# Performance work log

Measured on AMD Instinct MI355X. Metric: run time of the kernel, lower is better.

## Reference

```python
import jax, jax.numpy as jnp
import numpy as np

DIM = 1024
N_HEAD = 16
SEQ = 2048
GATE_IN = 12
ROPE_BASE = 10000.0
ATTN_SCALE = 0.1
EPS = 1e-6


def setup_inputs() -> dict:
    key = jax.random.key(0)
    ks = jax.random.split(key, 8)
    std = 0.5 * DIM ** -0.5
    bound = (3.0 ** 0.5) * std
    x = jax.random.normal(ks[0], (1, SEQ, DIM), dtype=jnp.float32)
    v1 = jax.random.normal(ks[1], (1, SEQ, DIM), dtype=jnp.float32)
    Wq = jax.random.uniform(ks[2], (DIM, DIM), jnp.float32, -bound, bound)
    Wk = jax.random.uniform(ks[3], (DIM, DIM), jnp.float32, -bound, bound)
    Wv = jax.random.uniform(ks[4], (DIM, DIM), jnp.float32, -bound, bound)
    # original zero-inits c_proj/attn_gate; use small random so output is non-trivial
    Wproj = jax.random.normal(ks[5], (DIM, DIM), dtype=jnp.float32) * 0.02
    Wgate = jax.random.normal(ks[6], (N_HEAD, GATE_IN), dtype=jnp.float32) * 0.02
    lamb = jnp.float32(0.5)
    return {"x": x, "v1": v1, "Wq": Wq, "Wk": Wk, "Wv": Wv,
            "Wproj": Wproj, "lamb": lamb, "Wgate": Wgate}


def _rms_norm(t):
    return t * jax.lax.rsqrt(jnp.mean(jnp.square(t), axis=-1, keepdims=True) + EPS)


def _rotary(t):
    # t: [B, T, H, hd]; rotates halves per the module's sign convention
    B, T, H, hd = t.shape
    d = hd // 2
    inv_freq = 1.0 / (ROPE_BASE ** (jnp.arange(0, hd, 2, dtype=jnp.float32) / hd))  # [d]
    freqs = jnp.arange(T, dtype=jnp.float32)[:, None] * inv_freq[None, :]  # [T, d]
    cos = jnp.cos(freqs)[None, :, None, :]
    sin = jnp.sin(freqs)[None, :, None, :]
    x1, x2 = t[..., :d], t[..., d:]
    y1 = x1 * cos + x2 * sin
    y2 = -x1 * sin + x2 * cos
    return jnp.concatenate([y1, y2], axis=-1)


def reference(x, v1, Wq, Wk, Wv, Wproj, lamb, Wgate):
    B, T, dim = x.shape
    H = Wgate.shape[0]
    hd = dim // H

    q = (x @ Wq.T).reshape(B, T, H, hd)
    k = (x @ Wk.T).reshape(B, T, H, hd)
    v = (x @ Wv.T).reshape(B, T, H, hd)

    # lambda-blended value mixing with residual value stream v1
    v = (1.0 - lamb) * v + lamb * v1.reshape(B, T, H, hd)

    q, k = _rms_norm(q), _rms_norm(k)
    q, k = _rotary(q), _rotary(k)

    # causal attention with fixed scale 0.1 (flex_attention block-sparse causal)
    scores = jnp.einsum("bthd,bshd->bhts", q, k) * ATTN_SCALE  # [B,H,T,T]
    causal = jnp.tril(jnp.ones((T, T), dtype=bool))
    scores = jnp.where(causal[None, None], scores, jnp.float32(-1e30))
    probs = jax.nn.softmax(scores, axis=-1)
    y = jnp.einsum("bhts,bshd->bthd", probs, v)  # [B,T,H,hd]

    # sigmoid gate from the first 12 channels of x, per head
    gate = jax.nn.sigmoid(x[..., :Wgate.shape[1]] @ Wgate.T)[..., None]  # [B,T,H,1]
    y = (y * gate).reshape(B, T, dim)
    y = y @ Wproj.T
    return y, v1
```

## Files before the change

kernel.cpp:

```cpp
#include <hip/hip_runtime.h>
#include <hip/hip_bf16.h>

#define T_SEQ 2048
#define NH 16
#define HD 64
#define SCALE_LOG2E 0.14426950408889634f

typedef __attribute__((ext_vector_type(8))) short bf16x8;
typedef __attribute__((ext_vector_type(4))) short bf16x4;
typedef __attribute__((ext_vector_type(4))) float f32x4;

__device__ __forceinline__ short f2bs(float f) {
  union { float f; unsigned u; } v; v.f = f;
  unsigned r = v.u + 0x7fffu + ((v.u >> 16) & 1u);
  return (short)(r >> 16);
}

__device__ __forceinline__ unsigned cvt_pk_bf16(float lo, float hi) {
  unsigned r;
  asm("v_cvt_pk_bf16_f32 %0, %1, %2" : "=v"(r) : "v"(lo), "v"(hi));
  return r;
}

__device__ __forceinline__ void gload16(const short* g, short* l) {
  __builtin_amdgcn_global_load_lds(
      (const __attribute__((address_space(1))) void*)g,
      (__attribute__((address_space(3))) void*)l, 16, 0, 0);
}

__global__ __launch_bounds__(256) void prep(const float* __restrict__ x,
                                            const float* __restrict__ wq,
                                            const float* __restrict__ wk,
                                            const float* __restrict__ wv,
                                            const float* __restrict__ wp,
                                            const float* __restrict__ v1,
                                            const float* __restrict__ Wg,
                                            short* __restrict__ xbT,
                                            short* __restrict__ wqkvT,
                                            short* __restrict__ wpjT,
                                            float* __restrict__ out2,
                                            float* __restrict__ gate,
                                            float2* __restrict__ rope) {
  const int rt = blockIdx.x;
  const int tid = threadIdx.x;
  if (blockIdx.y == 8) {
    int id = rt * 256 + tid;
    int t = id >> 4, h = id & 15;
    float acc = 0.f;
    #pragma unroll
    for (int i = 0; i < 12; ++i) acc += x[(size_t)t * 1024 + i] * Wg[h * 12 + i];
    gate[id] = 1.f / (1.f + __expf(-acc));
    #pragma unroll
    for (int j = 0; j < 2; ++j) {
      int e = id * 2 + j;
      int tt = e >> 5, p = e & 31;
      float invf = __builtin_exp2f(-0.41524101186092f * (float)p);
      float s, c;
      sincosf((float)tt * invf, &s, &c);
      rope[e] = make_float2(c, s);
    }
    return;
  }
  if (rt >= 96) {
    const int r0 = (rt - 96) * 64;
    const float* s = v1 + (size_t)r0 * 1024 + blockIdx.y * 128;
    float* d = out2 + (size_t)r0 * 1024 + blockIdx.y * 128;
    #pragma unroll
    for (int it = 0; it < 8; ++it) {
      int e = it * 256 + tid;
      int r = e >> 5, c4 = e & 31;
      *(float4*)&d[(size_t)r * 1024 + c4 * 4] = *(const float4*)&s[(size_t)r * 1024 + c4 * 4];
    }
    return;
  }
  __shared__ __attribute__((aligned(16))) short lv[64][136];
  const float* src; short* dst; int srow0, drow0, R;
  if (rt < 32)      { src = x;  dst = xbT;   R = 2048; srow0 = rt * 64;        drow0 = srow0; }
  else if (rt < 48) { src = wq; dst = wqkvT; R = 3072; srow0 = (rt - 32) * 64; drow0 = srow0; }
  else if (rt < 64) { src = wk; dst = wqkvT; R = 3072; srow0 = (rt - 48) * 64; drow0 = srow0 + 1024; }
  else if (rt < 80) { src = wv; dst = wqkvT; R = 3072; srow0 = (rt - 64) * 64; drow0 = srow0 + 2048; }
  else              { src = wp; dst = wpjT;  R = 1024; srow0 = (rt - 80) * 64; drow0 = srow0; }
  const int c0 = blockIdx.y * 16;
  #pragma unroll
  for (int it = 0; it < 8; ++it) {
    int e = it * 256 + tid;
    int r = e >> 5, c4 = e & 31;
    float4 v = *(const float4*)&src[(size_t)(srow0 + r) * 1024 + blockIdx.y * 128 + c4 * 4];
    bf16x4 o; o[0] = f2bs(v.x); o[1] = f2bs(v.y); o[2] = f2bs(v.z); o[3] = f2bs(v.w);
    *(bf16x4*)&lv[r][c4 * 4] = o;
  }
  __syncthreads();
  #pragma unroll
  for (int it = 0; it < 4; ++it) {
    int e = it * 256 + tid;
    int kc = e >> 6, r = e & 63;
    bf16x8 w = *(const bf16x8*)&lv[r][kc * 8];
    *(bf16x8*)&dst[((size_t)(c0 + kc) * R + drow0 + r) * 8] = w;
  }
}

template <int BM, bool QKV>
__global__ __launch_bounds__(256) void gemm(const short* __restrict__ A,
                                            const short* __restrict__ B,
                                            float* __restrict__ C,
                                            short* __restrict__ qb,
                                            short* __restrict__ kb,
                                            short* __restrict__ vt,
                                            const float* __restrict__ v1,
                                            const float* __restrict__ lambp,
                                            const float2* __restrict__ rope,
                                            int M, int N, int K) {
  constexpr int MF = BM / 32;
  constexpr int LA = BM / 64;
  __shared__ union {
    struct { short As[3][4][BM][8]; short Bs[3][4][128][8]; } g;
    short lv[128][130];
  } sm;
  const int tid = threadIdx.x;
  const int lane = tid & 63, wid = tid >> 6;
  const int lr = lane & 15, lg = lane >> 4;
  const int wm = (wid >> 1) * (BM / 2), wn = (wid & 1) * 64;
  const int bm = blockIdx.x * BM, bn = blockIdx.y * 128;
  const short* Ap = A + ((size_t)wid * M + bm + lane) * 8;
  const short* Bp = B + ((size_t)wid * N + bn + lane) * 8;
  f32x4 acc[MF][4] = {};
  auto stage = [&](int buf, int k0) {
    #pragma unroll
    for (int g = 0; g < LA; ++g)
      gload16(Ap + (size_t)k0 * M + g * 512, &sm.g.As[buf][wid][64 * g][0]);
    gload16(Bp + (size_t)k0 * N,       &sm.g.Bs[buf][wid][0][0]);
    gload16(Bp + (size_t)k0 * N + 512, &sm.g.Bs[buf][wid][64][0]);
  };
  auto compute = [&](int buf) {
    bf16x8 af[MF], bfr[4];
    #pragma unroll
    for (int m = 0; m < MF; ++m) af[m] = *(const bf16x8*)&sm.g.As[buf][lg][wm + m * 16 + lr][0];
    #pragma unroll
    for (int n = 0; n < 4; ++n) bfr[n] = *(const bf16x8*)&sm.g.Bs[buf][lg][wn + n * 16 + lr][0];
    #pragma unroll
    for (int m = 0; m < MF; ++m)
      #pragma unroll
      for (int n = 0; n < 4; ++n)
        acc[m][n] = __builtin_amdgcn_mfma_f32_16x16x32_bf16(af[m], bfr[n], acc[m][n], 0, 0, 0);
  };
  const int nsteps = K >> 5;
  stage(0, 0);
  stage(1, 32);
  int cur = 0;
  for (int ks = 0; ks < nsteps - 1; ++ks) {
    if constexpr (BM == 128) asm volatile("s_waitcnt vmcnt(4)" ::: "memory");
    else                     asm volatile("s_waitcnt vmcnt(3)" ::: "memory");
    __builtin_amdgcn_s_barrier();
    __builtin_amdgcn_sched_barrier(0);
    int s2 = cur + 2; if (s2 >= 3) s2 -= 3;
    if (ks + 2 < nsteps) stage(s2, (ks + 2) * 32);
    compute(cur);
    cur = (cur == 2) ? 0 : cur + 1;
  }
  asm volatile("s_waitcnt vmcnt(0)" ::: "memory");
  __builtin_amdgcn_s_barrier();
  __builtin_amdgcn_sched_barrier(0);
  compute(cur);

  if constexpr (QKV) {
    if (bn < 2048) {
      const bool isq = (bn < 1024);
      short* dst = isq ? qb : kb;
      const int h = ((bn + wn) & 1023) >> 6;
      #pragma unroll
      for (int m = 0; m < MF; ++m)
        #pragma unroll
        for (int r = 0; r < 4; ++r) {
          const int t = bm + wm + m * 16 + 4 * lg + r;
          float ss = acc[m][0][r] * acc[m][0][r] + acc[m][1][r] * acc[m][1][r]
                   + acc[m][2][r] * acc[m][2][r] + acc[m][3][r] * acc[m][3][r];
          ss += __shfl_xor(ss, 1);
          ss += __shfl_xor(ss, 2);
          ss += __shfl_xor(ss, 4);
          ss += __shfl_xor(ss, 8);
          const float rms = rsqrtf(ss * (1.f / 64.f) + 1e-6f);
          short* row = dst + ((size_t)h * T_SEQ + t) * 64;
          #pragma unroll
          for (int n2 = 0; n2 < 2; ++n2) {
            float x1 = acc[m][n2][r] * rms, x2 = acc[m][n2 + 2][r] * rms;
            float2 cs = rope[t * 32 + n2 * 16 + lr];
            float y1 = x1 * cs.x + x2 * cs.y;
            float y2 = x2 * cs.x - x1 * cs.y;
            if (isq) { y1 *= SCALE_LOG2E; y2 *= SCALE_LOG2E; }
            row[n2 * 16 + lr] = f2bs(y1);
            row[32 + n2 * 16 + lr] = f2bs(y2);
          }
        }
    } else {
      const float Lb = *lambp;
      const int h0 = (bn - 2048) >> 6;
      __syncthreads();
      #pragma unroll
      for (int m = 0; m < MF; ++m)
        #pragma unroll
        for (int r = 0; r < 4; ++r) {
          const int tl = wm + m * 16 + 4 * lg + r;
          const size_t vrow = (size_t)(bm + tl) * 1024 + h0 * 64;
          #pragma unroll
          for (int n = 0; n < 4; ++n) {
            const int col = wn + n * 16 + lr;
            float w = v1[vrow + col];
            sm.lv[tl][col] = f2bs((1.f - Lb) * acc[m][n][r] + Lb * w);
          }
        }
      __syncthreads();
      #pragma unroll
      for (int it = 0; it < 8; ++it) {
        int u = it * 256 + tid;
        int c0 = (u & 15) * 8;
        int d = (u >> 4) & 63;
        int hh = u >> 10;
        bf16x8 w;
        #pragma unroll
        for (int j = 0; j < 8; ++j) {
          int c = c0 + j;
          int src = (c & 96) | ((c & 1) << 4) | ((c >> 1) & 15);
          w[j] = sm.lv[src][hh * 64 + d];
        }
        *(bf16x8*)&vt[((size_t)(h0 + hh) * 64 + d) * T_SEQ + bm + c0] = w;
      }
    }
  } else {
    #pragma unroll
    for (int m = 0; m < MF; ++m)
      #pragma unroll
      for (int r = 0; r < 4; ++r) {
        const int t = bm + wm + m * 16 + 4 * lg + r;
        float* Cr = C + (size_t)t * N + bn + wn + lr;
        #pragma unroll
        for (int n = 0; n < 4; ++n) Cr[n * 16] = acc[m][n][r];
      }
  }
}

__global__ __launch_bounds__(256) void attn(const short* __restrict__ qb,
                                            const short* __restrict__ kb,
                                            const short* __restrict__ vtp,
                                            const float* __restrict__ gate,
                                            short* __restrict__ obT) {
  __shared__ __attribute__((aligned(16))) short Ks[2][4096];
  __shared__ __attribute__((aligned(16))) short Vs[2][4096];
  __shared__ __attribute__((aligned(16))) short p_lds[4][16][72];
  const int head = blockIdx.x & 15;
  const int qg = 31 - (blockIdx.x >> 4);
  const int nt = qg + 1;
  const int lane = threadIdx.x & 63, wid = threadIdx.x >> 6;
  const int lr = lane & 15, lg = lane >> 4;
  const int qt0 = qg * 64 + wid * 16;
  const short* Q = qb + (size_t)head * (T_SEQ * HD);
  const short* Kp = kb + (size_t)head * (T_SEQ * HD);
  const short* Vt = vtp + (size_t)head * (HD * T_SEQ);
  short (*P)[72] = p_lds[wid];

  bf16x8 aq0 = *(const bf16x8*)&Q[(size_t)(qt0 + lr) * HD + 8 * lg];
  bf16x8 aq1 = *(const bf16x8*)&Q[(size_t)(qt0 + lr) * HD + 32 + 8 * lg];
  f32x4 accO[4] = {};
  float lsum[4] = {0.f, 0.f, 0.f, 0.f};

  auto stage = [&](int buf, int jg) {
    const int kv0 = jg * 64;
    #pragma unroll
    for (int i = 0; i < 2; ++i) {
      int s = i * 256 + wid * 64 + lane;
      int row = s >> 3;
      int cG = (s & 7) ^ (row & 7);
      gload16(Kp + (size_t)(kv0 + row) * HD + cG * 8,
              &Ks[buf][(size_t)(i * 256 + wid * 64) * 8]);
      gload16(Vt + (size_t)row * T_SEQ + kv0 + cG * 8,
              &Vs[buf][(size_t)(i * 256 + wid * 64) * 8]);
    }
  };
  stage(0, 0);
  for (int j = 0; j < nt; ++j) {
    __syncthreads();
    if (j + 1 < nt) stage((j + 1) & 1, j + 1);
    const short* Kb = Ks[j & 1];
    const short* Vb = Vs[j & 1];
    f32x4 st[4];
    #pragma unroll
    for (int t = 0; t < 4; ++t) {
      int row = 16 * t + lr;
      int c0 = lg ^ (row & 7);
      bf16x8 k0 = *(const bf16x8*)&Kb[row * 64 + c0 * 8];
      bf16x8 k1 = *(const bf16x8*)&Kb[row * 64 + (c0 ^ 4) * 8];
      f32x4 s = {};
      s = __builtin_amdgcn_mfma_f32_16x16x32_bf16(aq0, k0, s, 0, 0, 0);
      s = __builtin_amdgcn_mfma_f32_16x16x32_bf16(aq1, k1, s, 0, 0, 0);
      st[t] = s;
    }
    if (j == qg) {
      #pragma unroll
      for (int t = 0; t < 4; ++t)
        #pragma unroll
        for (int r = 0; r < 4; ++r)
          st[t][r] = (16 * t + lr > wid * 16 + 4 * lg + r) ? -1e30f : st[t][r];
    }
    #pragma unroll
    for (int r = 0; r < 4; ++r) {
      float p0 = __builtin_exp2f(st[0][r]);
      float p1 = __builtin_exp2f(st[1][r]);
      float p2 = __builtin_exp2f(st[2][r]);
      float p3 = __builtin_exp2f(st[3][r]);
      lsum[r] += (p0 + p1) + (p2 + p3);
      *(unsigned*)&P[4 * lg + r][2 * lr] = cvt_pk_bf16(p0, p1);
      *(unsigned*)&P[4 * lg + r][32 + 2 * lr] = cvt_pk_bf16(p2, p3);
    }
    asm volatile("s_waitcnt lgkmcnt(0)" ::: "memory");
    __builtin_amdgcn_sched_barrier(0);
    bf16x8 pa0 = *(const bf16x8*)&P[lr][8 * lg];
    bf16x8 pa1 = *(const bf16x8*)&P[lr][32 + 8 * lg];
    #pragma unroll
    for (int nv = 0; nv < 4; ++nv) {
      int row0 = nv * 16 + lr;
      int c0 = lg ^ (row0 & 7);
      bf16x8 v0 = *(const bf16x8*)&Vb[row0 * 64 + c0 * 8];
      bf16x8 v1e = *(const bf16x8*)&Vb[row0 * 64 + (c0 ^ 4) * 8];
      accO[nv] = __builtin_amdgcn_mfma_f32_16x16x32_bf16(pa0, v0, accO[nv], 0, 0, 0);
      accO[nv] = __builtin_amdgcn_mfma_f32_16x16x32_bf16(pa1, v1e, accO[nv], 0, 0, 0);
    }
  }
  #pragma unroll
  for (int r = 0; r < 4; ++r) {
    float sres = lsum[r];
    sres += __shfl_xor(sres, 1);
    sres += __shfl_xor(sres, 2);
    sres += __shfl_xor(sres, 4);
    sres += __shfl_xor(sres, 8);
    const int t = qt0 + 4 * lg + r;
    const float gs = gate[t * 16 + head] / sres;
    #pragma unroll
    for (int nv = 0; nv < 4; ++nv) {
      const int col = nv * 16 + lr;
      obT[((size_t)(head * 8 + (col >> 3)) * T_SEQ + t) * 8 + (col & 7)] =
          f2bs(accO[nv][r] * gs);
    }
  }
}

extern "C" void kernel_launch(void* const* d_in, const int* in_sizes, int n_in,
                              void* d_out, int out_size, void* d_ws, size_t ws_size,
                              hipStream_t stream) {
  const float* x     = (const float*)d_in[0];
  const float* v1    = (const float*)d_in[1];
  const float* Wq    = (const float*)d_in[2];
  const float* Wk    = (const float*)d_in[3];
  const float* Wv    = (const float*)d_in[4];
  const float* Wproj = (const float*)d_in[5];
  const float* lamb  = (const float*)d_in[6];
  const float* Wgate = (const float*)d_in[7];
  float* out = (float*)d_out;

  char* ws = (char*)d_ws;
  short*  xbT   = (short*)(ws);
  short*  wqkvT = (short*)(ws + ((size_t)4  << 20));
  short*  wpjT  = (short*)(ws + ((size_t)10 << 20));
  float2* rope  = (float2*)(ws + ((size_t)34 << 20));
  short*  qb    = (short*)(ws + ((size_t)36 << 20));
  short*  kb    = (short*)(ws + ((size_t)40 << 20));
  short*  vt    = (short*)(ws + ((size_t)44 << 20));
  float*  gate  = (float*)(ws + ((size_t)48 << 20));
  short*  obT   = xbT;

  prep<<<dim3(128, 9), 256, 0, stream>>>(x, Wq, Wk, Wv, Wproj, v1, Wgate,
                                         xbT, wqkvT, wpjT,
                                         out + (size_t)T_SEQ * 1024, gate, rope);
  gemm<128, true><<<dim3(16, 24), 256, 0, stream>>>(xbT, wqkvT, nullptr, qb, kb, vt,
                                                    v1, lamb, rope, 2048, 3072, 1024);
  attn<<<512, 256, 0, stream>>>(qb, kb, vt, gate, obT);
  gemm<64, false><<<dim3(32, 8), 256, 0, stream>>>(obT, wpjT, out, nullptr, nullptr,
                                                   nullptr, nullptr, nullptr, nullptr,
                                                   2048, 1024, 1024);
}
```

Baseline: 82.97 us.

## Split causal attention along KV into strips with a separate reduce kernel

New measurement: 75.70 us. 1.1x faster.

```diff
diff --git a/kernel.cpp b/kernel.cpp
--- a/kernel.cpp
+++ b/kernel.cpp
@@ -14,6 +14,12 @@
   union { float f; unsigned u; } v; v.f = f;
   unsigned r = v.u + 0x7fffu + ((v.u >> 16) & 1u);
   return (short)(r >> 16);
+}
+
+__device__ __forceinline__ float bs2f(short s) {
+  union { unsigned u; float f; } v;
+  v.u = ((unsigned)(unsigned short)s) << 16;
+  return v.f;
 }
 
 __device__ __forceinline__ unsigned cvt_pk_bf16(float lo, float hi) {
@@ -241,14 +247,19 @@
 __global__ __launch_bounds__(256) void attn(const short* __restrict__ qb,
                                             const short* __restrict__ kb,
                                             const short* __restrict__ vtp,
-                                            const float* __restrict__ gate,
-                                            short* __restrict__ obT) {
+                                            short* __restrict__ partO,
+                                            float* __restrict__ partL) {
   __shared__ __attribute__((aligned(16))) short Ks[2][4096];
   __shared__ __attribute__((aligned(16))) short Vs[2][4096];
   __shared__ __attribute__((aligned(16))) short p_lds[4][16][72];
   const int head = blockIdx.x & 15;
-  const int qg = 31 - (blockIdx.x >> 4);
-  const int nt = qg + 1;
+  const int b = blockIdx.x >> 4;
+  int strip, qg;
+  if (b < 32)      { strip = 0; qg = 31 - b; }
+  else if (b < 56) { strip = 1; qg = 63 - b; }
+  else if (b < 72) { strip = 2; qg = 87 - b; }
+  else             { strip = 3; qg = 103 - b; }
+  const int nt = min(8, qg + 1 - strip * 8);
   const int lane = threadIdx.x & 63, wid = threadIdx.x >> 6;
   const int lr = lane & 15, lg = lane >> 4;
   const int qt0 = qg * 64 + wid * 16;
@@ -275,10 +286,11 @@
               &Vs[buf][(size_t)(i * 256 + wid * 64) * 8]);
     }
   };
-  stage(0, 0);
+  stage(0, strip * 8);
   for (int j = 0; j < nt; ++j) {
+    const int jg = strip * 8 + j;
     __syncthreads();
-    if (j + 1 < nt) stage((j + 1) & 1, j + 1);
+    if (j + 1 < nt) stage((j + 1) & 1, jg + 1);
     const short* Kb = Ks[j & 1];
     const short* Vb = Vs[j & 1];
     f32x4 st[4];
@@ -293,7 +305,7 @@
       s = __builtin_amdgcn_mfma_f32_16x16x32_bf16(aq1, k1, s, 0, 0, 0);
       st[t] = s;
     }
-    if (j == qg) {
+    if (jg == qg) {
       #pragma unroll
       for (int t = 0; t < 4; ++t)
         #pragma unroll
@@ -324,6 +336,8 @@
       accO[nv] = __builtin_amdgcn_mfma_f32_16x16x32_bf16(pa1, v1e, accO[nv], 0, 0, 0);
     }
   }
+  short* pO = partO + (size_t)(head * 80 + b) * 4096;
+  float* pL = partL + (size_t)(head * 80 + b) * 64;
   #pragma unroll
   for (int r = 0; r < 4; ++r) {
     float sres = lsum[r];
@@ -331,15 +345,50 @@
     sres += __shfl_xor(sres, 2);
     sres += __shfl_xor(sres, 4);
     sres += __shfl_xor(sres, 8);
-    const int t = qt0 + 4 * lg + r;
-    const float gs = gate[t * 16 + head] / sres;
-    #pragma unroll
-    for (int nv = 0; nv < 4; ++nv) {
-      const int col = nv * 16 + lr;
-      obT[((size_t)(head * 8 + (col >> 3)) * T_SEQ + t) * 8 + (col & 7)] =
-          f2bs(accO[nv][r] * gs);
-    }
-  }
+    int row = wid * 16 + 4 * lg + r;
+    #pragma unroll
+    for (int nv = 0; nv < 4; ++nv)
+      pO[row * 64 + nv * 16 + lr] = f2bs(accO[nv][r]);
+    if (lr == 0) pL[row] = sres;
+  }
+}
+
+__global__ __launch_bounds__(256) void attn_reduce(const short* __restrict__ partO,
+                                                   const float* __restrict__ partL,
+                                                   const float* __restrict__ gate,
+                                                   short* __restrict__ obT) {
+  const int head = blockIdx.x & 15;
+  const int qg = blockIdx.x >> 4;
+  const int ns = (qg >> 3) + 1;
+  const int tid = threadIdx.x;
+  const int row = tid >> 2, q4 = tid & 3;
+  const int sbase[4] = {0, 32, 56, 72};
+  f32x4 o[4] = {};
+  float l = 0.f;
+  for (int s = 0; s < ns; ++s) {
+    const int slot = head * 80 + sbase[s] + 31 - qg;
+    const short* pb = partO + (size_t)slot * 4096;
+    #pragma unroll
+    for (int c = 0; c < 4; ++c) {
+      bf16x4 v = *(const bf16x4*)&pb[row * 64 + q4 * 16 + c * 4];
+      #pragma unroll
+      for (int j = 0; j < 4; ++j) o[c][j] += bs2f(v[j]);
+    }
+    l += partL[(size_t)slot * 64 + row];
+  }
+  const int t = qg * 64 + row;
+  const float gs = gate[t * 16 + head] / l;
+  const int cg0 = head * 8 + q4 * 2;
+  bf16x8 w0, w1;
+  #pragma unroll
+  for (int j = 0; j < 4; ++j) {
+    w0[j]     = f2bs(o[0][j] * gs);
+    w0[4 + j] = f2bs(o[1][j] * gs);
+    w1[j]     = f2bs(o[2][j] * gs);
+    w1[4 + j] = f2bs(o[3][j] * gs);
+  }
+  *(bf16x8*)&obT[((size_t)cg0 * 2048 + t) * 8] = w0;
+  *(bf16x8*)&obT[((size_t)(cg0 + 1) * 2048 + t) * 8] = w1;
 }
 
 extern "C" void kernel_launch(void* const* d_in, const int* in_sizes, int n_in,
@@ -359,6 +408,8 @@
   short*  xbT   = (short*)(ws);
   short*  wqkvT = (short*)(ws + ((size_t)4  << 20));
   short*  wpjT  = (short*)(ws + ((size_t)10 << 20));
+  short*  partO = (short*)(ws + ((size_t)12 << 20));
+  float*  partL = (float*)(ws + ((size_t)23 << 20));
   float2* rope  = (float2*)(ws + ((size_t)34 << 20));
   short*  qb    = (short*)(ws + ((size_t)36 << 20));
   short*  kb    = (short*)(ws + ((size_t)40 << 20));
@@ -371,7 +422,8 @@
                                          out + (size_t)T_SEQ * 1024, gate, rope);
   gemm<128, true><<<dim3(16, 24), 256, 0, stream>>>(xbT, wqkvT, nullptr, qb, kb, vt,
                                                     v1, lamb, rope, 2048, 3072, 1024);
-  attn<<<512, 256, 0, stream>>>(qb, kb, vt, gate, obT);
+  attn<<<1280, 256, 0, stream>>>(qb, kb, vt, partO, partL);
+  attn_reduce<<<512, 256, 0, stream>>>(partO, partL, gate, obT);
   gemm<64, false><<<dim3(32, 8), 256, 0, stream>>>(obT, wpjT, out, nullptr, nullptr,
                                                    nullptr, nullptr, nullptr, nullptr,
                                                    2048, 1024, 1024);
```
